# Performance work log

Hardware: AMD Instinct MI355X
Metric: run time of the kernel (lower is better)

Reference implementation:

```python
import jax, jax.numpy as jnp
import numpy as np

TAU = 0.03        # self.tau
EPS = 0.65       # args.epsilon
EPS2 = 0.4       # args.epsilon2 (trimap)
LOGIT_T = 0.07    # logits temperature


def _l2norm(x, axis):
    # torch F.normalize: x / max(||x||, 1e-12)
    n = jnp.sqrt(jnp.sum(x * x, axis=axis, keepdims=True))
    return x / jnp.maximum(n, 1e-12)


def setup_inputs() -> dict:
    key = jax.random.key(0)
    k1, k2 = jax.random.split(key)
    img = jax.random.normal(k1, (256, 512, 14, 14), dtype=jnp.float32)
    aud = jax.random.normal(k2, (256, 512), dtype=jnp.float32)
    return {"img": img, "aud": aud}


def reference(img, aud):
    # img: [B, C, H, W] backbone vision features; aud: [B, C] pooled audio features
    B = img.shape[0]
    img = _l2norm(img, axis=1)
    aud = _l2norm(aud, axis=1)

    # A: paired audio-visual correlation map [B, 1, H, W]
    A = jnp.einsum('nchw,nc->nhw', img, aud)[:, None]
    # A0: full cross-pair correlation maps [B, B, H, W] (n = image idx, m = audio idx)
    A0 = jnp.einsum('nchw,mc->nmhw', img, aud)
    # AdaptiveMaxPool2d((1,1)) -> max over spatial dims -> [B, B]
    A0_ref = jnp.max(A0, axis=(2, 3))

    Pos = jax.nn.sigmoid((A - EPS) / TAU)           # [B, 1, H, W]
    Pos2 = jax.nn.sigmoid((A - EPS2) / TAU)         # trimap branch
    Neg = 1.0 - Pos2
    Pos_all = jax.nn.sigmoid((A0 - EPS) / TAU)      # [B, B, H, W]

    mask = 1.0 - 100.0 * jnp.eye(B, dtype=img.dtype)
    # gated weighted-mean pooling over spatial dims
    sim = (Pos_all * A0).sum(axis=(2, 3)) / Pos_all.sum(axis=(2, 3)) * mask   # [B, B]
    sim1 = (Pos * A).sum(axis=(2, 3)) / Pos.sum(axis=(2, 3))                  # [B, 1]
    sim2 = (Neg * A).sum(axis=(2, 3)) / Neg.sum(axis=(2, 3))                  # [B, 1]

    logits = jnp.concatenate((sim1, sim, sim2), axis=1) / LOGIT_T             # [B, B+2]
    return (A, logits, Pos, Neg, A0_ref)
```

## Files before the change

### kernel.cpp

```cpp
#include <hip/hip_runtime.h>
#include <math.h>

typedef _Float16 half8 __attribute__((ext_vector_type(8)));
typedef float f32x4 __attribute__((ext_vector_type(4)));

#define RLT (1.0f/0.07f)


__device__ __forceinline__ void gll16(const void* g, void* l) {
    __builtin_amdgcn_global_load_lds(
        (const __attribute__((address_space(1))) void*)g,
        (__attribute__((address_space(3))) void*)l, 16, 0, 0);
}

__global__ __launch_bounds__(256) void prep_aud_pk(const float* __restrict__ aud,
                                                   _Float16* __restrict__ aud_pk) {
    int m = blockIdx.x, t = threadIdx.x;
    float a0 = aud[m * 512 + t];
    float a1 = aud[m * 512 + 256 + t];
    float s = a0 * a0 + a1 * a1;
    #pragma unroll
    for (int off = 32; off; off >>= 1) s += __shfl_down(s, off, 64);
    __shared__ float wsum[4];
    __shared__ float rns;
    if ((t & 63) == 0) wsum[t >> 6] = s;
    __syncthreads();
    if (t == 0) rns = 1.0f / fmaxf(sqrtf(wsum[0] + wsum[1] + wsum[2] + wsum[3]), 1e-12f);
    __syncthreads();
    float rn = rns;
    int c0 = t, c1 = t + 256;
    aud_pk[(c0 >> 3) * 2048 + m * 8 + (c0 & 7)] = (_Float16)(a0 * rn);
    aud_pk[(c1 >> 3) * 2048 + m * 8 + (c1 & 7)] = (_Float16)(a1 * rn);
}

__global__ __launch_bounds__(512, 4) void av_ovl(const float* __restrict__ img,
                                                 const _Float16* __restrict__ aud_pk,
                                                 float* __restrict__ out,
                                                 float* __restrict__ pmax,
                                                 float* __restrict__ psw,
                                                 float* __restrict__ pswa,
                                                 float* __restrict__ pdiag) {
    const int bid = blockIdx.x;
    const int n = bid >> 1, half = bid & 1;
    const int tid = threadIdx.x;
    const int w = tid >> 6, l = tid & 63;
    const int q = w & 3;
    const int hg = w >> 2;
    const int HT = hg ? 3 : 4;

    __shared__ _Float16 __align__(16) Abuf[2][4][112][8];
    __shared__ _Float16 __align__(16) Bbuf[2][4][256][8];
    __shared__ float nrm_parts[4][98];
    __shared__ float rnorm_s[112];
    __shared__ float red_max[2][256], red_sw[2][256], red_swa[2][256];
    __shared__ float diag_parts[2][4][4];

    if (tid < 112) {
        int b = tid / 56, rem = tid % 56, kg = rem / 14, row = 98 + rem % 14;
        *(float4*)&Abuf[b][kg][row][0] = make_float4(0.f, 0.f, 0.f, 0.f);
    }

    const float* imgn = img + (size_t)n * (512 * 196);
    const bool act = tid < 392;
    const int p   = act ? tid / 98 : 0;
    const int hwl = act ? tid % 98 : 0;
    const int g   = half * 98 + hwl;
    float nrm = 0.f;
    float av0[8], av1[8];

    #define STAGE_B(t, buf)                                                         \
        do {                                                                        \
            const _Float16* g0 = aud_pk + (((size_t)(t) * 1024 + w * 64 + l) << 3); \
            _Float16* l0 = &Bbuf[buf][0][0][0] + ((w * 64) << 3);                   \
            gll16(g0, l0);                                                          \
            gll16(g0 + 4096, l0 + 4096);                                            \
        } while (0)

    #define LOAD_A_TO(dst, t)                                                       \
        do {                                                                        \
            const float* src = imgn + ((size_t)(32 * (t) + p * 8)) * 196 + g;       \
            _Pragma("unroll")                                                       \
            for (int i = 0; i < 8; i++) dst[i] = src[i * 196];                      \
            asm volatile("" :: "v"(dst[0]), "v"(dst[1]), "v"(dst[2]), "v"(dst[3]),  \
                               "v"(dst[4]), "v"(dst[5]), "v"(dst[6]), "v"(dst[7])); \
        } while (0)

    #define STAGE_A_FROM(srcv, buf)                                                 \
        do {                                                                        \
            if (act) {                                                              \
                half8 h0;                                                           \
                _Pragma("unroll")                                                   \
                for (int i = 0; i < 8; i++) {                                       \
                    h0[i] = (_Float16)srcv[i];                                      \
                    nrm += srcv[i] * srcv[i];                                       \
                }                                                                   \
                *(half8*)&Abuf[buf][p][hwl][0] = h0;                                \
            }                                                                       \
        } while (0)

    STAGE_B(0, 0);
    asm volatile("" ::: "memory");
    LOAD_A_TO(av0, 0);
    asm volatile("" ::: "memory");
    LOAD_A_TO(av1, 1);
    asm volatile("" ::: "memory");
    STAGE_A_FROM(av0, 0);
    asm volatile("s_waitcnt lgkmcnt(0)" ::: "memory");
    asm volatile("s_waitcnt vmcnt(8)" ::: "memory");
    __builtin_amdgcn_s_barrier();
    __builtin_amdgcn_sched_barrier(0);

    f32x4 acc[4][4];
    #pragma unroll
    for (int ht = 0; ht < 4; ht++)
        #pragma unroll
        for (int mt = 0; mt < 4; mt++)
            acc[ht][mt] = (f32x4){0.f, 0.f, 0.f, 0.f};

    const int kk = l >> 4, lm = l & 15;
    const int aoff = kk * 896  + (hg * 64 + lm) * 8;
    const int boff = kk * 2048 + (q * 64 + lm) * 8;

    #define STEP(t, cur, loadSlot, stageSlot)                                       \
        do {                                                                        \
            const int nb_ = (cur) ^ 1;                                              \
            if ((t) <= 14) STAGE_B((t) + 1, nb_);                                   \
            asm volatile("" ::: "memory");                                          \
            if ((t) <= 13) LOAD_A_TO(loadSlot, (t) + 2);                            \
            asm volatile("" ::: "memory");                                          \
            {                                                                       \
                const _Float16* Ab = &Abuf[cur][0][0][0];                           \
                const _Float16* Bb = &Bbuf[cur][0][0][0];                           \
                half8 afrag[4];                                                     \
                _Pragma("unroll")                                                   \
                for (int ht = 0; ht < 4; ht++)                                      \
                    if (ht < HT) afrag[ht] = *(const half8*)(Ab + aoff + ht * 128); \
                __builtin_amdgcn_s_setprio(1);                                      \
                _Pragma("unroll")                                                   \
                for (int mt = 0; mt < 4; mt++) {                                    \
                    half8 bfrag = *(const half8*)(Bb + boff + mt * 128);            \
                    _Pragma("unroll")                                               \
                    for (int ht = 0; ht < 4; ht++)                                  \
                        if (ht < HT)                                                \
                            acc[ht][mt] = __builtin_amdgcn_mfma_f32_16x16x32_f16(   \
                                afrag[ht], bfrag, acc[ht][mt], 0, 0, 0);            \
                }                                                                   \
                __builtin_amdgcn_s_setprio(0);                                      \
            }                                                                       \
            __builtin_amdgcn_sched_barrier(0);                                      \
            if ((t) <= 14) STAGE_A_FROM(stageSlot, nb_);                            \
            if ((t) < 15) {                                                         \
                asm volatile("s_waitcnt lgkmcnt(0)" ::: "memory");                  \
                if ((t) <= 13) asm volatile("s_waitcnt vmcnt(8)" ::: "memory");     \
                else           asm volatile("s_waitcnt vmcnt(0)" ::: "memory");     \
                __builtin_amdgcn_s_barrier();                                       \
                __builtin_amdgcn_sched_barrier(0);                                  \
            }                                                                       \
        } while (0)

    #pragma unroll
    for (int tt = 0; tt < 16; tt += 2) {
        STEP(tt,     0, av0, av1);
        STEP(tt + 1, 1, av1, av0);
    }

    #undef STEP
    #undef STAGE_B
    #undef LOAD_A_TO
    #undef STAGE_A_FROM

    if (act) nrm_parts[p][hwl] = nrm;
    __syncthreads();
    if (tid < 112) {
        float v = 0.f;
        if (tid < 98)
            v = 1.0f / fmaxf(sqrtf(nrm_parts[0][tid] + nrm_parts[1][tid] +
                                   nrm_parts[2][tid] + nrm_parts[3][tid]), 1e-12f);
        rnorm_s[tid] = v;
    }
    __syncthreads();

    float mx[4], sw[4], swa[4];
    #pragma unroll
    for (int mt = 0; mt < 4; mt++) { mx[mt] = -1e30f; sw[mt] = 0.f; swa[mt] = 0.f; }
    float s1n = 0.f, s1d = 0.f, s2n = 0.f, s2d = 0.f;
    const int dmt = (n >> 4) & 3, dq = n >> 6, dl = n & 15;
    const bool isdiag = (q == dq) && (lm == dl);

    #pragma unroll
    for (int ht = 0; ht < 4; ht++) {
        if (ht < HT) {
            int rowb = hg * 64 + ht * 16 + (kk << 2);
            #pragma unroll
            for (int r = 0; r < 4; r++) {
                int row = rowb + r;
                float rn = rnorm_s[row];
                bool valid = row < 98;
                int hw = half * 98 + row;
                #pragma unroll
                for (int mt = 0; mt < 4; mt++) {
                    float a0 = acc[ht][mt][r] * rn;
                    if (valid) {
                        float wg = 1.0f / (1.0f + __expf((0.65f - a0) * (1.0f / 0.03f)));
                        mx[mt]  = fmaxf(mx[mt], a0);
                        sw[mt] += wg;
                        swa[mt] += wg * a0;
                        if (isdiag && mt == dmt) {
                            out[n * 196 + hw] = a0;
                            out[116224 + n * 196 + hw] = wg;
                            float p2 = 1.0f / (1.0f + __expf((0.40f - a0) * (1.0f / 0.03f)));
                            float ng = 1.0f - p2;
                            out[166400 + n * 196 + hw] = ng;
                            s1n += wg * a0; s1d += wg;
                            s2n += ng * a0; s2d += ng;
                        }
                    }
                }
            }
        }
    }

    #pragma unroll
    for (int mt = 0; mt < 4; mt++) {
        float m1 = mx[mt], v1 = sw[mt], v2 = swa[mt];
        m1 = fmaxf(m1, __shfl_xor(m1, 16, 64)); v1 += __shfl_xor(v1, 16, 64); v2 += __shfl_xor(v2, 16, 64);
        m1 = fmaxf(m1, __shfl_xor(m1, 32, 64)); v1 += __shfl_xor(v1, 32, 64); v2 += __shfl_xor(v2, 32, 64);
        if (l < 16) {
            int m = q * 64 + mt * 16 + l;
            red_max[hg][m] = m1; red_sw[hg][m] = v1; red_swa[hg][m] = v2;
        }
    }
    if (isdiag) {
        diag_parts[hg][kk][0] = s1n;
        diag_parts[hg][kk][1] = s1d;
        diag_parts[hg][kk][2] = s2n;
        diag_parts[hg][kk][3] = s2d;
    }
    __syncthreads();

    if (tid < 256) {
        int m = tid;
        int base = (n * 2 + half) * 256 + m;
        pmax[base] = fmaxf(red_max[0][m], red_max[1][m]);
        psw[base]  = red_sw[0][m] + red_sw[1][m];
        pswa[base] = red_swa[0][m] + red_swa[1][m];
    }
    if (tid < 4) {
        float s = 0.f;
        #pragma unroll
        for (int h2 = 0; h2 < 2; h2++)
            #pragma unroll
            for (int lg = 0; lg < 4; lg++)
                s += diag_parts[h2][lg][tid];
        pdiag[(n * 2 + half) * 4 + tid] = s;
    }
}

__global__ __launch_bounds__(256) void av_final(const float* __restrict__ pmax,
                                                const float* __restrict__ psw,
                                                const float* __restrict__ pswa,
                                                const float* __restrict__ pdiag,
                                                float* __restrict__ out) {
    int n = blockIdx.x, m = threadIdx.x;
    int b0 = (n * 2) * 256 + m, b1 = (n * 2 + 1) * 256 + m;
    float mx = fmaxf(pmax[b0], pmax[b1]);
    float sim = (pswa[b0] + pswa[b1]) / (psw[b0] + psw[b1]);
    if (m == n) sim *= -99.0f;
    out[50176 + n * 258 + 1 + m] = sim * RLT;
    out[216576 + n * 256 + m] = mx;
    if (m == n) {
        const float* d = pdiag + n * 8;
        out[50176 + n * 258]       = ((d[0] + d[4]) / (d[1] + d[5])) * RLT;
        out[50176 + n * 258 + 257] = ((d[2] + d[6]) / (d[3] + d[7])) * RLT;
    }
}

extern "C" void kernel_launch(void* const* d_in, const int* in_sizes, int n_in,
                              void* d_out, int out_size, void* d_ws, size_t ws_size,
                              hipStream_t stream) {
    const float* img = (const float*)d_in[0];
    const float* aud = (const float*)d_in[1];
    float* out = (float*)d_out;

    _Float16* aud_pk = (_Float16*)d_ws;
    float* wsf   = (float*)d_ws;
    float* pmax  = wsf + 65536;
    float* psw   = pmax + 131072;
    float* pswa  = psw + 131072;
    float* pdiag = pswa + 131072;

    prep_aud_pk<<<256, 256, 0, stream>>>(aud, aud_pk);
    av_ovl<<<512, 512, 0, stream>>>(img, aud_pk, out, pmax, psw, pswa, pdiag);
    av_final<<<256, 256, 0, stream>>>(pmax, psw, pswa, pdiag, out);
}
```

Before: 44.30 us.

## Process full spatial map per block and fuse final reduction into main kernel

Each block now handles an entire image (all 196 spatial positions) rather than half of one. This removes the cross-block partial sums and the separate av_final kernel, and sim, max and diagonal logits are written directly from shared memory. Each thread loads 16 channels per step and keeps 7x4 accumulators, so the grid halves to 256 blocks and register pressure rises (launch bounds now 2 blocks per CU). This trades one kernel launch and workspace traffic for fewer, heavier blocks, which may reduce occupancy and latency hiding on a 256-CU part.

Result: slower. 50.08 us (median of 2 runs) (+13.0%).

```diff
diff --git a/kernel.cpp b/kernel.cpp
--- a/kernel.cpp
+++ b/kernel.cpp
@@ -33,44 +33,39 @@
     aud_pk[(c1 >> 3) * 2048 + m * 8 + (c1 & 7)] = (_Float16)(a1 * rn);
 }
 
-__global__ __launch_bounds__(512, 4) void av_ovl(const float* __restrict__ img,
+__global__ __launch_bounds__(512, 2) void av_one(const float* __restrict__ img,
                                                  const _Float16* __restrict__ aud_pk,
-                                                 float* __restrict__ out,
-                                                 float* __restrict__ pmax,
-                                                 float* __restrict__ psw,
-                                                 float* __restrict__ pswa,
-                                                 float* __restrict__ pdiag) {
-    const int bid = blockIdx.x;
-    const int n = bid >> 1, half = bid & 1;
+                                                 float* __restrict__ out) {
+    const int n = blockIdx.x;
     const int tid = threadIdx.x;
     const int w = tid >> 6, l = tid & 63;
     const int q = w & 3;
-    const int hg = w >> 2;
-    const int HT = hg ? 3 : 4;
-
-    __shared__ _Float16 __align__(16) Abuf[2][4][112][8];
+    const int hh = w >> 2;
+    const int HT = hh ? 6 : 7;
+    const int kk = l >> 4, lm = l & 15;
+
+    __shared__ _Float16 __align__(16) Abuf[2][4][208][8];
     __shared__ _Float16 __align__(16) Bbuf[2][4][256][8];
-    __shared__ float nrm_parts[4][98];
-    __shared__ float rnorm_s[112];
+    __shared__ float nrm_parts[2][196];
+    __shared__ float rnorm_s[208];
     __shared__ float red_max[2][256], red_sw[2][256], red_swa[2][256];
     __shared__ float diag_parts[2][4][4];
 
-    if (tid < 112) {
-        int b = tid / 56, rem = tid % 56, kg = rem / 14, row = 98 + rem % 14;
+    if (tid < 96) {
+        int b = tid / 48, rem = tid % 48, kg = rem / 12, row = 196 + rem % 12;
         *(float4*)&Abuf[b][kg][row][0] = make_float4(0.f, 0.f, 0.f, 0.f);
     }
 
     const float* imgn = img + (size_t)n * (512 * 196);
     const bool act = tid < 392;
-    const int p   = act ? tid / 98 : 0;
-    const int hwl = act ? tid % 98 : 0;
-    const int g   = half * 98 + hwl;
+    const int p   = act ? tid / 196 : 0;
+    const int hwl = act ? tid % 196 : 0;
     float nrm = 0.f;
-    float av0[8], av1[8];
+    float av0[16], av1[16];
 
     #define STAGE_B(t, buf)                                                         \
         do {                                                                        \
-            const _Float16* g0 = aud_pk + (((size_t)(t) * 1024 + w * 64 + l) << 3); \
+            const _Float16* g0 = aud_pk + (((size_t)(t) * 1024 + tid) << 3);        \
             _Float16* l0 = &Bbuf[buf][0][0][0] + ((w * 64) << 3);                   \
             gll16(g0, l0);                                                          \
             gll16(g0 + 4096, l0 + 4096);                                            \
@@ -78,23 +73,27 @@
 
     #define LOAD_A_TO(dst, t)                                                       \
         do {                                                                        \
-            const float* src = imgn + ((size_t)(32 * (t) + p * 8)) * 196 + g;       \
+            const float* src = imgn + ((size_t)(32 * (t) + p * 16)) * 196 + hwl;    \
             _Pragma("unroll")                                                       \
-            for (int i = 0; i < 8; i++) dst[i] = src[i * 196];                      \
+            for (int i = 0; i < 16; i++) dst[i] = src[i * 196];                     \
             asm volatile("" :: "v"(dst[0]), "v"(dst[1]), "v"(dst[2]), "v"(dst[3]),  \
                                "v"(dst[4]), "v"(dst[5]), "v"(dst[6]), "v"(dst[7])); \
+            asm volatile("" :: "v"(dst[8]), "v"(dst[9]), "v"(dst[10]), "v"(dst[11]),\
+                               "v"(dst[12]), "v"(dst[13]), "v"(dst[14]), "v"(dst[15])); \
         } while (0)
 
     #define STAGE_A_FROM(srcv, buf)                                                 \
         do {                                                                        \
             if (act) {                                                              \
-                half8 h0;                                                           \
+                half8 h0, h1;                                                       \
                 _Pragma("unroll")                                                   \
                 for (int i = 0; i < 8; i++) {                                       \
                     h0[i] = (_Float16)srcv[i];                                      \
-                    nrm += srcv[i] * srcv[i];                                       \
+                    h1[i] = (_Float16)srcv[8 + i];                                  \
+                    nrm += srcv[i] * srcv[i] + srcv[8 + i] * srcv[8 + i];           \
                 }                                                                   \
-                *(half8*)&Abuf[buf][p][hwl][0] = h0;                                \
+                *(half8*)&Abuf[buf][2 * p][hwl][0]     = h0;                        \
+                *(half8*)&Abuf[buf][2 * p + 1][hwl][0] = h1;                        \
             }                                                                       \
         } while (0)
 
@@ -102,23 +101,20 @@
     asm volatile("" ::: "memory");
     LOAD_A_TO(av0, 0);
     asm volatile("" ::: "memory");
+    STAGE_A_FROM(av0, 0);
     LOAD_A_TO(av1, 1);
-    asm volatile("" ::: "memory");
-    STAGE_A_FROM(av0, 0);
     asm volatile("s_waitcnt lgkmcnt(0)" ::: "memory");
-    asm volatile("s_waitcnt vmcnt(8)" ::: "memory");
     __builtin_amdgcn_s_barrier();
     __builtin_amdgcn_sched_barrier(0);
 
-    f32x4 acc[4][4];
-    #pragma unroll
-    for (int ht = 0; ht < 4; ht++)
+    f32x4 acc[7][4];
+    #pragma unroll
+    for (int ht = 0; ht < 7; ht++)
         #pragma unroll
         for (int mt = 0; mt < 4; mt++)
             acc[ht][mt] = (f32x4){0.f, 0.f, 0.f, 0.f};
 
-    const int kk = l >> 4, lm = l & 15;
-    const int aoff = kk * 896  + (hg * 64 + lm) * 8;
+    const int aoff = kk * 1664 + (hh * 112 + lm) * 8;
     const int boff = kk * 2048 + (q * 64 + lm) * 8;
 
     #define STEP(t, cur, loadSlot, stageSlot)                                       \
@@ -131,16 +127,16 @@
             {                                                                       \
                 const _Float16* Ab = &Abuf[cur][0][0][0];                           \
                 const _Float16* Bb = &Bbuf[cur][0][0][0];                           \
-                half8 afrag[4];                                                     \
+                half8 afrag[7];                                                     \
                 _Pragma("unroll")                                                   \
-                for (int ht = 0; ht < 4; ht++)                                      \
+                for (int ht = 0; ht < 7; ht++)                                      \
                     if (ht < HT) afrag[ht] = *(const half8*)(Ab + aoff + ht * 128); \
                 __builtin_amdgcn_s_setprio(1);                                      \
                 _Pragma("unroll")                                                   \
                 for (int mt = 0; mt < 4; mt++) {                                    \
                     half8 bfrag = *(const half8*)(Bb + boff + mt * 128);            \
                     _Pragma("unroll")                                               \
-                    for (int ht = 0; ht < 4; ht++)                                  \
+                    for (int ht = 0; ht < 7; ht++)                                  \
                         if (ht < HT)                                                \
                             acc[ht][mt] = __builtin_amdgcn_mfma_f32_16x16x32_f16(   \
                                 afrag[ht], bfrag, acc[ht][mt], 0, 0, 0);            \
@@ -151,7 +147,7 @@
             if ((t) <= 14) STAGE_A_FROM(stageSlot, nb_);                            \
             if ((t) < 15) {                                                         \
                 asm volatile("s_waitcnt lgkmcnt(0)" ::: "memory");                  \
-                if ((t) <= 13) asm volatile("s_waitcnt vmcnt(8)" ::: "memory");     \
+                if ((t) <= 13) asm volatile("s_waitcnt vmcnt(16)" ::: "memory");    \
                 else           asm volatile("s_waitcnt vmcnt(0)" ::: "memory");     \
                 __builtin_amdgcn_s_barrier();                                       \
                 __builtin_amdgcn_sched_barrier(0);                                  \
@@ -171,11 +167,10 @@
 
     if (act) nrm_parts[p][hwl] = nrm;
     __syncthreads();
-    if (tid < 112) {
+    if (tid < 208) {
         float v = 0.f;
-        if (tid < 98)
-            v = 1.0f / fmaxf(sqrtf(nrm_parts[0][tid] + nrm_parts[1][tid] +
-                                   nrm_parts[2][tid] + nrm_parts[3][tid]), 1e-12f);
+        if (tid < 196)
+            v = 1.0f / fmaxf(sqrtf(nrm_parts[0][tid] + nrm_parts[1][tid]), 1e-12f);
         rnorm_s[tid] = v;
     }
     __syncthreads();
@@ -188,15 +183,14 @@
     const bool isdiag = (q == dq) && (lm == dl);
 
     #pragma unroll
-    for (int ht = 0; ht < 4; ht++) {
+    for (int ht = 0; ht < 7; ht++) {
         if (ht < HT) {
-            int rowb = hg * 64 + ht * 16 + (kk << 2);
+            int rowb = hh * 112 + ht * 16 + (kk << 2);
             #pragma unroll
             for (int r = 0; r < 4; r++) {
-                int row = rowb + r;
-                float rn = rnorm_s[row];
-                bool valid = row < 98;
-                int hw = half * 98 + row;
+                int hw = rowb + r;
+                float rn = rnorm_s[hw];
+                bool valid = hw < 196;
                 #pragma unroll
                 for (int mt = 0; mt < 4; mt++) {
                     float a0 = acc[ht][mt][r] * rn;
@@ -227,51 +221,38 @@
         m1 = fmaxf(m1, __shfl_xor(m1, 32, 64)); v1 += __shfl_xor(v1, 32, 64); v2 += __shfl_xor(v2, 32, 64);
         if (l < 16) {
             int m = q * 64 + mt * 16 + l;
-            red_max[hg][m] = m1; red_sw[hg][m] = v1; red_swa[hg][m] = v2;
+            red_max[hh][m] = m1; red_sw[hh][m] = v1; red_swa[hh][m] = v2;
         }
     }
     if (isdiag) {
-        diag_parts[hg][kk][0] = s1n;
-        diag_parts[hg][kk][1] = s1d;
-        diag_parts[hg][kk][2] = s2n;
-        diag_parts[hg][kk][3] = s2d;
+        diag_parts[hh][kk][0] = s1n;
+        diag_parts[hh][kk][1] = s1d;
+        diag_parts[hh][kk][2] = s2n;
+        diag_parts[hh][kk][3] = s2d;
     }
     __syncthreads();
 
     if (tid < 256) {
         int m = tid;
-        int base = (n * 2 + half) * 256 + m;
-        pmax[base] = fmaxf(red_max[0][m], red_max[1][m]);
-        psw[base]  = red_sw[0][m] + red_sw[1][m];
-        pswa[base] = red_swa[0][m] + red_swa[1][m];
-    }
-    if (tid < 4) {
-        float s = 0.f;
-        #pragma unroll
-        for (int h2 = 0; h2 < 2; h2++)
+        float mxv = fmaxf(red_max[0][m], red_max[1][m]);
+        float num = red_swa[0][m] + red_swa[1][m];
+        float den = red_sw[0][m] + red_sw[1][m];
+        float sim = num / den;
+        if (m == n) sim *= -99.0f;
+        out[50176 + n * 258 + 1 + m] = sim * RLT;
+        out[216576 + n * 256 + m] = mxv;
+        if (m == n) {
+            float t1n = 0.f, t1d = 0.f, t2n = 0.f, t2d = 0.f;
             #pragma unroll
-            for (int lg = 0; lg < 4; lg++)
-                s += diag_parts[h2][lg][tid];
-        pdiag[(n * 2 + half) * 4 + tid] = s;
-    }
-}
-
-__global__ __launch_bounds__(256) void av_final(const float* __restrict__ pmax,
-                                                const float* __restrict__ psw,
-                                                const float* __restrict__ pswa,
-                                                const float* __restrict__ pdiag,
-                                                float* __restrict__ out) {
-    int n = blockIdx.x, m = threadIdx.x;
-    int b0 = (n * 2) * 256 + m, b1 = (n * 2 + 1) * 256 + m;
-    float mx = fmaxf(pmax[b0], pmax[b1]);
-    float sim = (pswa[b0] + pswa[b1]) / (psw[b0] + psw[b1]);
-    if (m == n) sim *= -99.0f;
-    out[50176 + n * 258 + 1 + m] = sim * RLT;
-    out[216576 + n * 256 + m] = mx;
-    if (m == n) {
-        const float* d = pdiag + n * 8;
-        out[50176 + n * 258]       = ((d[0] + d[4]) / (d[1] + d[5])) * RLT;
-        out[50176 + n * 258 + 257] = ((d[2] + d[6]) / (d[3] + d[7])) * RLT;
+            for (int h2 = 0; h2 < 2; h2++)
+                #pragma unroll
+                for (int g2 = 0; g2 < 4; g2++) {
+                    t1n += diag_parts[h2][g2][0]; t1d += diag_parts[h2][g2][1];
+                    t2n += diag_parts[h2][g2][2]; t2d += diag_parts[h2][g2][3];
+                }
+            out[50176 + n * 258]       = (t1n / t1d) * RLT;
+            out[50176 + n * 258 + 257] = (t2n / t2d) * RLT;
+        }
     }
 }
 
@@ -281,15 +262,8 @@
     const float* img = (const float*)d_in[0];
     const float* aud = (const float*)d_in[1];
     float* out = (float*)d_out;
-
     _Float16* aud_pk = (_Float16*)d_ws;
-    float* wsf   = (float*)d_ws;
-    float* pmax  = wsf + 65536;
-    float* psw   = pmax + 131072;
-    float* pswa  = psw + 131072;
-    float* pdiag = pswa + 131072;
 
     prep_aud_pk<<<256, 256, 0, stream>>>(aud, aud_pk);
-    av_ovl<<<512, 512, 0, stream>>>(img, aud_pk, out, pmax, psw, pswa, pdiag);
-    av_final<<<256, 256, 0, stream>>>(pmax, psw, pswa, pdiag, out);
-}
+    av_one<<<256, 512, 0, stream>>>(img, aud_pk, out);
+}
```
